# Kernel tuning notes

Hardware: AMD Instinct MI355X
Metric: run time of the kernel (lower is better)

## Reference

```python
import jax, jax.numpy as jnp
from jax import lax
import numpy as np

DIM = 384
NUM_HEADS = 8
HEAD_DIM = DIM // NUM_HEADS


def setup_inputs() -> dict:
    key = jax.random.key(0)
    k_x, k_qw, k_qb, k_lw, k_lb = jax.random.split(key, 5)
    B, H, W = 2, 64, 64
    N = H * W
    x = jax.random.normal(k_x, (B, N, DIM), dtype=jnp.float32)
    # nn.Linear(dim, 3*dim): weight (3C, C), bias (3C,)
    qkv_w = jax.random.normal(k_qw, (3 * DIM, DIM), dtype=jnp.float32) * (1.0 / np.sqrt(DIM))
    qkv_b = jax.random.normal(k_qb, (3 * DIM,), dtype=jnp.float32) * 0.02
    # nn.Conv2d(dim, dim, 3, padding=1, groups=dim): weight (C, 1, 3, 3), bias (C,)
    lepe_w = jax.random.normal(k_lw, (DIM, 1, 3, 3), dtype=jnp.float32) * (1.0 / 3.0)
    lepe_b = jax.random.normal(k_lb, (DIM,), dtype=jnp.float32) * 0.02
    return {"x": x, "qkv_w": qkv_w, "qkv_b": qkv_b, "lepe_w": lepe_w, "lepe_b": lepe_b, "H": H, "W": W}


def reference(x, qkv_w, qkv_b, lepe_w, lepe_b, H, W):
    B, N, C = x.shape
    hd = C // NUM_HEADS
    scale = hd ** -0.5
    # qkv projection: (B, N, 3C) -> (B, N, 3, heads, head_dim)
    qkv = (jnp.einsum('bnc,oc->bno', x, qkv_w) + qkv_b).reshape(B, N, 3, NUM_HEADS, hd)
    q, k, v = qkv[:, :, 0], qkv[:, :, 1], qkv[:, :, 2]  # each (B, N, heads, hd)
    attn = jnp.einsum('bnhd,bmhd->bhnm', q * scale, k)   # (B, heads, N, N)
    attn = jax.nn.softmax(attn, axis=-1)
    out = jnp.einsum('bhnm,bmhd->bnhd', attn, v).reshape(B, N, C)
    # LePE: depthwise 3x3 conv on v in NCHW layout
    v_img = v.reshape(B, H, W, C).transpose(0, 3, 1, 2)  # (B, C, H, W)
    lepe = lax.conv_general_dilated(
        v_img, lepe_w, window_strides=(1, 1), padding='SAME',
        feature_group_count=C,
        dimension_numbers=('NCHW', 'OIHW', 'NCHW'))
    lepe = lepe + lepe_b[None, :, None, None]
    return out + lepe.transpose(0, 2, 3, 1).reshape(B, N, C)
```

## Files before the change

### kernel.cpp

```cpp
#include <hip/hip_runtime.h>
#include <stdint.h>

#define DIM   384
#define NH    8
#define HD    48
#define NTOK  4096
#define KDIM  384
#define SCALEL2E 0.20823509610f

typedef float  f32x4   __attribute__((ext_vector_type(4)));
typedef float  f32x16  __attribute__((ext_vector_type(16)));
typedef __bf16 bf16x8  __attribute__((ext_vector_type(8)));

#if __has_builtin(__builtin_amdgcn_exp2f)
#define EXP2F(x) __builtin_amdgcn_exp2f(x)
#else
#define EXP2F(x) exp2f(x)
#endif

__device__ __forceinline__ unsigned short f2bf(float f) {
  union { float f; unsigned int u; } c; c.f = f;
  unsigned int r = (c.u + 0x7FFFu + ((c.u >> 16) & 1u)) >> 16;
  return (unsigned short)r;
}
__device__ __forceinline__ float bf2f(unsigned short h) {
  union { unsigned int u; float f; } c; c.u = ((unsigned int)h) << 16;
  return c.f;
}


__global__ void prep_kernel(const float* __restrict__ x, const float* __restrict__ w,
                            unsigned short* __restrict__ x_bf,
                            unsigned short* __restrict__ w_bf) {
  int tid = blockIdx.x * blockDim.x + threadIdx.x;
  int stride = gridDim.x * blockDim.x;
  for (int i = tid; i < 786432; i += stride) {
    float4 v = ((const float4*)x)[i];
    ushort4 o;
    o.x = f2bf(v.x); o.y = f2bf(v.y); o.z = f2bf(v.z); o.w = f2bf(v.w);
    ((ushort4*)x_bf)[i] = o;
  }
  for (int i = tid; i < 110592; i += stride) {
    float4 v = ((const float4*)w)[i];
    ushort4 o;
    o.x = f2bf(v.x); o.y = f2bf(v.y); o.z = f2bf(v.z); o.w = f2bf(v.w);
    ((ushort4*)w_bf)[i] = o;
  }
}

__global__ __launch_bounds__(256) void qkv_gemm(
    const unsigned short* __restrict__ A,
    const unsigned short* __restrict__ Bw,
    const float* __restrict__ bias,
    unsigned short* __restrict__ qc,
    unsigned short* __restrict__ kc,
    unsigned short* __restrict__ v_t) {
  __shared__ unsigned short ldsA[128 * 32];
  __shared__ unsigned short ldsB[64 * 32];
  __shared__ unsigned short ebuf[64 * 72];
  const int tid = threadIdx.x;
  const int wv = tid >> 6, ln = tid & 63;
  const int lrow = ln & 15, lq = ln >> 4;
  const int m0 = blockIdx.x * 128;
  const int n0 = blockIdx.y * 64;
  const int wm = (wv >> 1) * 64, wn = (wv & 1) * 32;

  f32x4 acc[4][2];
#pragma unroll
  for (int mi = 0; mi < 4; ++mi)
#pragma unroll
    for (int ni = 0; ni < 2; ++ni)
#pragma unroll
      for (int r = 0; r < 4; ++r) acc[mi][ni][r] = 0.f;

  for (int k0 = 0; k0 < KDIM; k0 += 32) {
    __syncthreads();
#pragma unroll
    for (int j = 0; j < 2; ++j) {
      int r16 = wv * 2 + j;
      const unsigned short* ga = A + (size_t)(m0 + r16 * 16 + (ln >> 2)) * KDIM
                                   + k0 + (ln & 3) * 8;
      __builtin_amdgcn_global_load_lds(
          (const __attribute__((address_space(1))) void*)ga,
          (__attribute__((address_space(3))) void*)&ldsA[r16 * 512], 16, 0, 0);
    }
    const unsigned short* gb = Bw + (size_t)(n0 + wv * 16 + (ln >> 2)) * KDIM
                                  + k0 + (ln & 3) * 8;
    __builtin_amdgcn_global_load_lds(
        (const __attribute__((address_space(1))) void*)gb,
        (__attribute__((address_space(3))) void*)&ldsB[wv * 512], 16, 0, 0);
    __syncthreads();
    bf16x8 af[4], bfv[2];
#pragma unroll
    for (int mi = 0; mi < 4; ++mi)
      af[mi] = *(const bf16x8*)&ldsA[(wm + mi * 16 + lrow) * 32 + lq * 8];
#pragma unroll
    for (int ni = 0; ni < 2; ++ni)
      bfv[ni] = *(const bf16x8*)&ldsB[(wn + ni * 16 + lrow) * 32 + lq * 8];
#pragma unroll
    for (int mi = 0; mi < 4; ++mi)
#pragma unroll
      for (int ni = 0; ni < 2; ++ni)
        acc[mi][ni] = __builtin_amdgcn_mfma_f32_16x16x32_bf16(
            af[mi], bfv[ni], acc[mi][ni], 0, 0, 0);
  }

  const int region = (n0 >= 768) ? 2 : (n0 >= 384 ? 1 : 0);
  const float scl = (region == 0) ? SCALEL2E : 1.0f;
  const float bias0 = bias[n0 + wn + lrow];
  const float bias1 = bias[n0 + wn + 16 + lrow];

#pragma unroll
  for (int half = 0; half < 2; ++half) {
    __syncthreads();
    if ((wv >> 1) == half) {
#pragma unroll
      for (int mi = 0; mi < 4; ++mi)
#pragma unroll
        for (int ni = 0; ni < 2; ++ni)
#pragma unroll
          for (int r = 0; r < 4; ++r) {
            int row = mi * 16 + lq * 4 + r;
            int col = wn + ni * 16 + lrow;
            float val = (acc[mi][ni][r] + (ni ? bias1 : bias0)) * scl;
            ebuf[row * 72 + col] = f2bf(val);
          }
    }
    __syncthreads();
    if (region < 2) {
      unsigned short* dst = (region == 0) ? qc : kc;
      const int obase = n0 - region * 384;
#pragma unroll
      for (int i = 0; i < 2; ++i) {
        int id = tid + i * 256;
        int row = id >> 3, cc = id & 7;
        uint4 val = *(const uint4*)&ebuf[row * 72 + cc * 8];
        int nrow = m0 + half * 64 + row;
        int b = nrow >> 12, nn = nrow & 4095;
        int o = obase + cc * 8;
        int h = o / 48, d = o - h * 48;
        *(uint4*)&dst[((size_t)(b * 8 + h) * NTOK + nn) * HD + d] = val;
      }
    } else {
#pragma unroll
      for (int i = 0; i < 2; ++i) {
        int id = tid + i * 256;
        int col = id & 63, rc = id >> 6;
        int r0 = rc * 8;
        ushort4 lo, hi;
        lo.x = ebuf[(r0 + 0) * 72 + col]; lo.y = ebuf[(r0 + 1) * 72 + col];
        lo.z = ebuf[(r0 + 2) * 72 + col]; lo.w = ebuf[(r0 + 3) * 72 + col];
        hi.x = ebuf[(r0 + 4) * 72 + col]; hi.y = ebuf[(r0 + 5) * 72 + col];
        hi.z = ebuf[(r0 + 6) * 72 + col]; hi.w = ebuf[(r0 + 7) * 72 + col];
        uint4 pk;
        pk.x = (unsigned int)lo.x | ((unsigned int)lo.y << 16);
        pk.y = (unsigned int)lo.z | ((unsigned int)lo.w << 16);
        pk.z = (unsigned int)hi.x | ((unsigned int)hi.y << 16);
        pk.w = (unsigned int)hi.z | ((unsigned int)hi.w << 16);
        int nrow = m0 + half * 64 + r0;
        int b = nrow >> 12;
        int o = n0 - 768 + col;
        *(uint4*)&v_t[((size_t)(b * DIM + o)) * NTOK + (nrow & 4095)] = pk;
      }
    }
  }
}

__global__ __launch_bounds__(256) void lepe_kernel(
    const unsigned short* __restrict__ v_t,
    const float* __restrict__ lw, const float* __restrict__ lb,
    float* __restrict__ out) {
  __shared__ __align__(16) unsigned short pl[16 * 648];
  const int cg = blockIdx.x;
  const int sy = blockIdx.y;
  const int b  = blockIdx.z;
  const int t = threadIdx.x;
  const int y0 = sy * 8;
#pragma unroll
  for (int i = 0; i < 5; ++i) {
    int id = t + i * 256;
    int c = id / 80, rem = id - c * 80;
    int row = rem >> 3, cx = rem & 7;
    int y = y0 - 1 + row;
    uint4 val = make_uint4(0u, 0u, 0u, 0u);
    if (y >= 0 && y < 64)
      val = *(const uint4*)(v_t + ((size_t)(b * DIM + cg * 16 + c)) * NTOK + y * 64 + cx * 8);
    *(uint4*)&pl[c * 648 + row * 64 + cx * 8] = val;
  }
  __syncthreads();
  const int c = t & 15, pg = t >> 4;
  const int cglob = cg * 16 + c;
  float w[9];
#pragma unroll
  for (int j = 0; j < 9; ++j) w[j] = lw[cglob * 9 + j];
  const float bias = lb[cglob];
  const unsigned short* base = &pl[c * 648];
  for (int i = 0; i < 32; ++i) {
    int p = pg * 32 + i;
    int lr = p >> 6, x = p & 63;
    float acc = bias;
#pragma unroll
    for (int ky = 0; ky < 3; ++ky)
#pragma unroll
      for (int kx = 0; kx < 3; ++kx) {
        int xx = x + kx - 1;
        if (xx >= 0 && xx < 64)
          acc += w[ky * 3 + kx] * bf2f(base[(lr + ky) * 64 + xx]);
      }
    out[((size_t)(b * NTOK + sy * 512 + p)) * DIM + cglob] = acc;
  }
}

__global__ __launch_bounds__(256, 2) void attn_kernel(
    const unsigned short* __restrict__ qc,
    const unsigned short* __restrict__ kcg,
    const unsigned short* __restrict__ v_t,
    float* __restrict__ out) {
  __shared__ __align__(16) char smem[36864];
  unsigned short* Kl = (unsigned short*)smem;
  unsigned short* Vl = (unsigned short*)(smem + 18432);
  float* Lsum = (float*)(smem + 35840);
  float* Ol   = (float*)smem;

  const int tid = threadIdx.x;
  const int wv = tid >> 6, ln = tid & 63;
  const int kh = wv >> 1;
  const int wq = wv & 1;
  const int l31 = ln & 31, hh = ln >> 5;
  const int th = tid & 127;
  const int qb = blockIdx.x;
  const int bh = blockIdx.y;
  const int b = bh >> 3, hd = bh & 7;

  unsigned short* Kh = Kl + kh * 4608;
  unsigned short* Vh = Vl + kh * 4352;

  int kwo[4], kgo[4], vwo[3], vgo[3];
#pragma unroll
  for (int i = 0; i < 4; ++i) {
    int idx = th + i * 128;
    int r = idx >> 3, cc = idx & 7;
    kwo[i] = r * 72 + cc * 8;
    kgo[i] = r * 48 + cc * 8;
  }
#pragma unroll
  for (int i = 0; i < 3; ++i) {
    int idx = th + i * 128;
    int vd = idx >> 3, vc = idx & 7;
    vwo[i] = vd * 68 + vc * 8;
    vgo[i] = vd * 4096 + vc * 8;
  }

  if (th < 8) {
    uint4 one4 = make_uint4(0x3F803F80u, 0x3F803F80u, 0x3F803F80u, 0x3F803F80u);
    *(uint4*)&Vh[48 * 68 + th * 8] = one4;
  }

  bf16x8 Qf[2][3];
#pragma unroll
  for (int set = 0; set < 2; ++set) {
    const int qrow = qb * 128 + set * 64 + wq * 32 + l31;
    const unsigned short* qp = qc + ((size_t)bh * NTOK + qrow) * HD + hh * 8;
#pragma unroll
    for (int hs = 0; hs < 3; ++hs)
      Qf[set][hs] = *(const bf16x8*)(qp + hs * 16);
  }

  f32x16 Oacc[2][2];
#pragma unroll
  for (int set = 0; set < 2; ++set)
#pragma unroll
    for (int dc = 0; dc < 2; ++dc)
#pragma unroll
      for (int r = 0; r < 16; ++r) Oacc[set][dc][r] = 0.f;

  const unsigned short* kbase = kcg + (size_t)bh * NTOK * HD;
  const unsigned short* vbase = v_t + ((size_t)b * DIM + hd * HD) * NTOK;

  uint4 kreg0, kreg1, kreg2, kreg3, vreg0, vreg1, vreg2;
  {
    const unsigned short* kg = kbase + (size_t)(kh * 32) * 64 * HD;
    const unsigned short* vg = vbase + (kh * 32) * 64;
    kreg0 = *(const uint4*)(kg + kgo[0]);
    kreg1 = *(const uint4*)(kg + kgo[1]);
    kreg2 = *(const uint4*)(kg + kgo[2]);
    kreg3 = *(const uint4*)(kg + kgo[3]);
    vreg0 = *(const uint4*)(vg + vgo[0]);
    vreg1 = *(const uint4*)(vg + vgo[1]);
    vreg2 = *(const uint4*)(vg + vgo[2]);
  }

  for (int it = 0; it < 32; ++it) {
    __syncthreads();
    *(uint4*)&Kh[kwo[0]] = kreg0;
    *(uint4*)&Kh[kwo[1]] = kreg1;
    *(uint4*)&Kh[kwo[2]] = kreg2;
    *(uint4*)&Kh[kwo[3]] = kreg3;
    *(uint4*)&Vh[vwo[0]] = vreg0;
    *(uint4*)&Vh[vwo[1]] = vreg1;
    *(uint4*)&Vh[vwo[2]] = vreg2;
    {
      int ktn = kh * 32 + ((it + 1) & 31);
      const unsigned short* kg = kbase + (size_t)ktn * 64 * HD;
      const unsigned short* vg = vbase + ktn * 64;
      kreg0 = *(const uint4*)(kg + kgo[0]);
      kreg1 = *(const uint4*)(kg + kgo[1]);
      kreg2 = *(const uint4*)(kg + kgo[2]);
      kreg3 = *(const uint4*)(kg + kgo[3]);
      vreg0 = *(const uint4*)(vg + vgo[0]);
      vreg1 = *(const uint4*)(vg + vgo[1]);
      vreg2 = *(const uint4*)(vg + vgo[2]);
    }
    __syncthreads();

#pragma unroll
    for (int C = 0; C < 2; ++C) {
      f32x16 sA, sB;
#pragma unroll
      for (int r = 0; r < 16; ++r) { sA[r] = 0.f; sB[r] = 0.f; }
      const unsigned short* kr = &Kh[(C * 32 + l31) * 72 + hh * 8];
#pragma unroll
      for (int hs = 0; hs < 3; ++hs) {
        bf16x8 kf = *(const bf16x8*)(kr + hs * 16);
        sA = __builtin_amdgcn_mfma_f32_32x32x16_bf16(kf, Qf[0][hs], sA, 0, 0, 0);
        sB = __builtin_amdgcn_mfma_f32_32x32x16_bf16(kf, Qf[1][hs], sB, 0, 0, 0);
      }
      unsigned int PA[8], PB[8];
#pragma unroll
      for (int t8 = 0; t8 < 8; ++t8) {
        float a0 = EXP2F(sA[2 * t8]);
        float a1 = EXP2F(sA[2 * t8 + 1]);
        PA[t8] = __builtin_amdgcn_perm(__float_as_uint(a1), __float_as_uint(a0),
                                       0x07060302u);
        float b0 = EXP2F(sB[2 * t8]);
        float b1 = EXP2F(sB[2 * t8 + 1]);
        PB[t8] = __builtin_amdgcn_perm(__float_as_uint(b1), __float_as_uint(b0),
                                       0x07060302u);
      }
#pragma unroll
      for (int u = 0; u < 2; ++u) {
        bf16x8 pav0 = __builtin_bit_cast(bf16x8,
            make_uint4(PA[4 * u + 0], PA[4 * u + 1], PA[4 * u + 2], PA[4 * u + 3]));
        bf16x8 pav1 = __builtin_bit_cast(bf16x8,
            make_uint4(PB[4 * u + 0], PB[4 * u + 1], PB[4 * u + 2], PB[4 * u + 3]));
        const int goff = (C * 8 + 4 * u + hh) * 4;
#pragma unroll
        for (int dc = 0; dc < 2; ++dc) {
          const int vrow = dc * 32 + l31;
          const unsigned short* vrp = &Vh[vrow * 68 + goff];
          uint2 g0 = *(const uint2*)(vrp);
          uint2 g2 = *(const uint2*)(vrp + 8);
          bf16x8 vfv = __builtin_bit_cast(bf16x8, make_uint4(g0.x, g0.y, g2.x, g2.y));
          Oacc[0][dc] = __builtin_amdgcn_mfma_f32_32x32x16_bf16(
              pav0, vfv, Oacc[0][dc], 0, 0, 0);
          Oacc[1][dc] = __builtin_amdgcn_mfma_f32_32x32x16_bf16(
              pav1, vfv, Oacc[1][dc], 0, 0, 0);
        }
      }
    }
  }

  __syncthreads();
  if (l31 == 16) {
#pragma unroll
    for (int set = 0; set < 2; ++set)
#pragma unroll
      for (int r = 0; r < 16; ++r) {
        int qrb = set * 64 + wq * 32 + (r & 3) + 8 * (r >> 2) + 4 * hh;
        Lsum[kh * 128 + qrb] = Oacc[set][1][r];
      }
  }
  if (kh == 1) {
#pragma unroll
    for (int set = 0; set < 2; ++set)
#pragma unroll
      for (int r = 0; r < 16; ++r) {
        int qrb = set * 64 + wq * 32 + (r & 3) + 8 * (r >> 2) + 4 * hh;
        Ol[qrb * 48 + l31] = Oacc[set][0][r];
        if (l31 < 16) Ol[qrb * 48 + 32 + l31] = Oacc[set][1][r];
      }
  }
  __syncthreads();
  if (kh == 0) {
#pragma unroll
    for (int set = 0; set < 2; ++set)
#pragma unroll
      for (int r = 0; r < 16; ++r) {
        int qrb = set * 64 + wq * 32 + (r & 3) + 8 * (r >> 2) + 4 * hh;
        float linv = 1.0f / (Lsum[qrb] + Lsum[128 + qrb]);
        float* op = out + ((size_t)(b * NTOK + qb * 128 + qrb)) * DIM + hd * HD;
        op[l31] += (Oacc[set][0][r] + Ol[qrb * 48 + l31]) * linv;
        if (l31 < 16)
          op[32 + l31] += (Oacc[set][1][r] + Ol[qrb * 48 + 32 + l31]) * linv;
      }
  }
}

extern "C" void kernel_launch(void* const* d_in, const int* in_sizes, int n_in,
                              void* d_out, int out_size, void* d_ws, size_t ws_size,
                              hipStream_t stream) {
  const float* x      = (const float*)d_in[0];
  const float* qkv_w  = (const float*)d_in[1];
  const float* qkv_b  = (const float*)d_in[2];
  const float* lepe_w = (const float*)d_in[3];
  const float* lepe_b = (const float*)d_in[4];

  char* ws = (char*)d_ws;
  unsigned short* x_bf = (unsigned short*)(ws);
  unsigned short* w_bf = (unsigned short*)(ws + 6291456);
  unsigned short* qcp  = (unsigned short*)(ws + 7176192);
  unsigned short* kcp  = (unsigned short*)(ws + 13467648);
  unsigned short* v_t  = (unsigned short*)(ws + 19759104);
  float* out = (float*)d_out;

  prep_kernel<<<1024, 256, 0, stream>>>(x, qkv_w, x_bf, w_bf);
  qkv_gemm<<<dim3(64, 18), 256, 0, stream>>>(x_bf, w_bf, qkv_b, qcp, kcp, v_t);
  lepe_kernel<<<dim3(24, 8, 2), 256, 0, stream>>>(v_t, lepe_w, lepe_b, out);
  attn_kernel<<<dim3(32, 16), 256, 0, stream>>>(qcp, kcp, v_t, out);
}
```

Baseline: 188.4 us.

## Split attention KV range across four waves with private LDS tiles

Each attention block now covers 64 queries instead of 128, and the key range is split four ways, one slice per wave. Each wave stages its own 32-key K/V tiles in private LDS, so the per-iteration block barriers are gone. The K tile uses an XOR swizzle to reduce bank conflicts. Row sums now come from accumulating the fp32 exponentials in registers instead of the ones-column MFMA trick, and the four partial outputs are reduced through LDS at the end. The grid doubles and launch bounds ask for 3 blocks per CU. The cost is twice the K/V traffic through L2, plus an extra LDS reduction stage.

```diff
diff --git a/kernel.cpp b/kernel.cpp
--- a/kernel.cpp
+++ b/kernel.cpp
@@ -211,55 +211,45 @@
   }
 }
 
-__global__ __launch_bounds__(256, 2) void attn_kernel(
+__global__ __launch_bounds__(256, 3) void attn_kernel(
     const unsigned short* __restrict__ qc,
     const unsigned short* __restrict__ kcg,
     const unsigned short* __restrict__ v_t,
     float* __restrict__ out) {
-  __shared__ __align__(16) char smem[36864];
+  __shared__ __align__(16) char smem[33056];
   unsigned short* Kl = (unsigned short*)smem;
-  unsigned short* Vl = (unsigned short*)(smem + 18432);
-  float* Lsum = (float*)(smem + 35840);
-  float* Ol   = (float*)smem;
+  unsigned short* Vl = (unsigned short*)(smem + 16384);
+  float* Lsum = (float*)(smem + 32032);
+  float* bufA = (float*)smem;
+  float* bufB = (float*)(smem + 12288);
 
   const int tid = threadIdx.x;
-  const int wv = tid >> 6, ln = tid & 63;
-  const int kh = wv >> 1;
-  const int wq = wv & 1;
+  const int kh = tid >> 6;
+  const int ln = tid & 63;
   const int l31 = ln & 31, hh = ln >> 5;
-  const int th = tid & 127;
   const int qb = blockIdx.x;
   const int bh = blockIdx.y;
   const int b = bh >> 3, hd = bh & 7;
 
-  unsigned short* Kh = Kl + kh * 4608;
-  unsigned short* Vh = Vl + kh * 4352;
-
-  int kwo[4], kgo[4], vwo[3], vgo[3];
-#pragma unroll
-  for (int i = 0; i < 4; ++i) {
-    int idx = th + i * 128;
-    int r = idx >> 3, cc = idx & 7;
-    kwo[i] = r * 72 + cc * 8;
+  unsigned short* Kh = Kl + kh * 2048;
+  unsigned short* Vh = Vl + kh * 1764;
+
+  int kwo[3], kgo[3], vwo[3], vgo[3];
+#pragma unroll
+  for (int i = 0; i < 3; ++i) {
+    int idx = ln + i * 64;
+    int r = idx / 6, cc = idx - r * 6;
+    kwo[i] = r * 64 + ((cc ^ (r & 7)) * 8);
     kgo[i] = r * 48 + cc * 8;
-  }
-#pragma unroll
-  for (int i = 0; i < 3; ++i) {
-    int idx = th + i * 128;
-    int vd = idx >> 3, vc = idx & 7;
-    vwo[i] = vd * 68 + vc * 8;
-    vgo[i] = vd * 4096 + vc * 8;
-  }
-
-  if (th < 8) {
-    uint4 one4 = make_uint4(0x3F803F80u, 0x3F803F80u, 0x3F803F80u, 0x3F803F80u);
-    *(uint4*)&Vh[48 * 68 + th * 8] = one4;
+    int vd = idx >> 2, c4 = idx & 3;
+    vwo[i] = vd * 36 + c4 * 8;
+    vgo[i] = vd * 4096 + c4 * 8;
   }
 
   bf16x8 Qf[2][3];
 #pragma unroll
   for (int set = 0; set < 2; ++set) {
-    const int qrow = qb * 128 + set * 64 + wq * 32 + l31;
+    const int qrow = qb * 64 + set * 32 + l31;
     const unsigned short* qp = qc + ((size_t)bh * NTOK + qrow) * HD + hh * 8;
 #pragma unroll
     for (int hs = 0; hs < 3; ++hs)
@@ -273,112 +263,122 @@
     for (int dc = 0; dc < 2; ++dc)
 #pragma unroll
       for (int r = 0; r < 16; ++r) Oacc[set][dc][r] = 0.f;
+  float lsum0 = 0.f, lsum1 = 0.f;
 
   const unsigned short* kbase = kcg + (size_t)bh * NTOK * HD;
   const unsigned short* vbase = v_t + ((size_t)b * DIM + hd * HD) * NTOK;
 
-  uint4 kreg0, kreg1, kreg2, kreg3, vreg0, vreg1, vreg2;
+  uint4 kr0, kr1, kr2, vr0, vr1, vr2;
   {
-    const unsigned short* kg = kbase + (size_t)(kh * 32) * 64 * HD;
-    const unsigned short* vg = vbase + (kh * 32) * 64;
-    kreg0 = *(const uint4*)(kg + kgo[0]);
-    kreg1 = *(const uint4*)(kg + kgo[1]);
-    kreg2 = *(const uint4*)(kg + kgo[2]);
-    kreg3 = *(const uint4*)(kg + kgo[3]);
-    vreg0 = *(const uint4*)(vg + vgo[0]);
-    vreg1 = *(const uint4*)(vg + vgo[1]);
-    vreg2 = *(const uint4*)(vg + vgo[2]);
+    const unsigned short* kg = kbase + (size_t)(kh * 32) * 32 * HD;
+    const unsigned short* vg = vbase + (kh * 32) * 32;
+    kr0 = *(const uint4*)(kg + kgo[0]);
+    kr1 = *(const uint4*)(kg + kgo[1]);
+    kr2 = *(const uint4*)(kg + kgo[2]);
+    vr0 = *(const uint4*)(vg + vgo[0]);
+    vr1 = *(const uint4*)(vg + vgo[1]);
+    vr2 = *(const uint4*)(vg + vgo[2]);
   }
 
   for (int it = 0; it < 32; ++it) {
-    __syncthreads();
-    *(uint4*)&Kh[kwo[0]] = kreg0;
-    *(uint4*)&Kh[kwo[1]] = kreg1;
-    *(uint4*)&Kh[kwo[2]] = kreg2;
-    *(uint4*)&Kh[kwo[3]] = kreg3;
-    *(uint4*)&Vh[vwo[0]] = vreg0;
-    *(uint4*)&Vh[vwo[1]] = vreg1;
-    *(uint4*)&Vh[vwo[2]] = vreg2;
+    *(uint4*)&Kh[kwo[0]] = kr0;
+    *(uint4*)&Kh[kwo[1]] = kr1;
+    *(uint4*)&Kh[kwo[2]] = kr2;
+    *(uint4*)&Vh[vwo[0]] = vr0;
+    *(uint4*)&Vh[vwo[1]] = vr1;
+    *(uint4*)&Vh[vwo[2]] = vr2;
     {
       int ktn = kh * 32 + ((it + 1) & 31);
-      const unsigned short* kg = kbase + (size_t)ktn * 64 * HD;
-      const unsigned short* vg = vbase + ktn * 64;
-      kreg0 = *(const uint4*)(kg + kgo[0]);
-      kreg1 = *(const uint4*)(kg + kgo[1]);
-      kreg2 = *(const uint4*)(kg + kgo[2]);
-      kreg3 = *(const uint4*)(kg + kgo[3]);
-      vreg0 = *(const uint4*)(vg + vgo[0]);
-      vreg1 = *(const uint4*)(vg + vgo[1]);
-      vreg2 = *(const uint4*)(vg + vgo[2]);
-    }
-    __syncthreads();
-
-#pragma unroll
-    for (int C = 0; C < 2; ++C) {
-      f32x16 sA, sB;
-#pragma unroll
-      for (int r = 0; r < 16; ++r) { sA[r] = 0.f; sB[r] = 0.f; }
-      const unsigned short* kr = &Kh[(C * 32 + l31) * 72 + hh * 8];
-#pragma unroll
-      for (int hs = 0; hs < 3; ++hs) {
-        bf16x8 kf = *(const bf16x8*)(kr + hs * 16);
-        sA = __builtin_amdgcn_mfma_f32_32x32x16_bf16(kf, Qf[0][hs], sA, 0, 0, 0);
-        sB = __builtin_amdgcn_mfma_f32_32x32x16_bf16(kf, Qf[1][hs], sB, 0, 0, 0);
+      const unsigned short* kg = kbase + (size_t)ktn * 32 * HD;
+      const unsigned short* vg = vbase + ktn * 32;
+      kr0 = *(const uint4*)(kg + kgo[0]);
+      kr1 = *(const uint4*)(kg + kgo[1]);
+      kr2 = *(const uint4*)(kg + kgo[2]);
+      vr0 = *(const uint4*)(vg + vgo[0]);
+      vr1 = *(const uint4*)(vg + vgo[1]);
+      vr2 = *(const uint4*)(vg + vgo[2]);
+    }
+
+    f32x16 sA, sB;
+#pragma unroll
+    for (int r = 0; r < 16; ++r) { sA[r] = 0.f; sB[r] = 0.f; }
+    const unsigned short* kr = &Kh[l31 * 64];
+    const int rx = l31 & 7;
+#pragma unroll
+    for (int hs = 0; hs < 3; ++hs) {
+      bf16x8 kf = *(const bf16x8*)&kr[((hs * 2 + hh) ^ rx) * 8];
+      sA = __builtin_amdgcn_mfma_f32_32x32x16_bf16(kf, Qf[0][hs], sA, 0, 0, 0);
+      sB = __builtin_amdgcn_mfma_f32_32x32x16_bf16(kf, Qf[1][hs], sB, 0, 0, 0);
+    }
+    unsigned int PA[8], PB[8];
+#pragma unroll
+    for (int t8 = 0; t8 < 8; ++t8) {
+      float a0 = EXP2F(sA[2 * t8]);
+      float a1 = EXP2F(sA[2 * t8 + 1]);
+      lsum0 += a0 + a1;
+      PA[t8] = __builtin_amdgcn_perm(__float_as_uint(a1), __float_as_uint(a0),
+                                     0x07060302u);
+      float b0 = EXP2F(sB[2 * t8]);
+      float b1 = EXP2F(sB[2 * t8 + 1]);
+      lsum1 += b0 + b1;
+      PB[t8] = __builtin_amdgcn_perm(__float_as_uint(b1), __float_as_uint(b0),
+                                     0x07060302u);
+    }
+#pragma unroll
+    for (int u = 0; u < 2; ++u) {
+      bf16x8 pav0 = __builtin_bit_cast(bf16x8,
+          make_uint4(PA[4 * u + 0], PA[4 * u + 1], PA[4 * u + 2], PA[4 * u + 3]));
+      bf16x8 pav1 = __builtin_bit_cast(bf16x8,
+          make_uint4(PB[4 * u + 0], PB[4 * u + 1], PB[4 * u + 2], PB[4 * u + 3]));
+      const int goff = (4 * u + hh) * 4;
+#pragma unroll
+      for (int dc = 0; dc < 2; ++dc) {
+        const int vrow = dc * 32 + l31;
+        const unsigned short* vrp = &Vh[vrow * 36 + goff];
+        uint2 g0 = *(const uint2*)(vrp);
+        uint2 g2 = *(const uint2*)(vrp + 8);
+        bf16x8 vfv = __builtin_bit_cast(bf16x8, make_uint4(g0.x, g0.y, g2.x, g2.y));
+        Oacc[0][dc] = __builtin_amdgcn_mfma_f32_32x32x16_bf16(
+            pav0, vfv, Oacc[0][dc], 0, 0, 0);
+        Oacc[1][dc] = __builtin_amdgcn_mfma_f32_32x32x16_bf16(
+            pav1, vfv, Oacc[1][dc], 0, 0, 0);
       }
-      unsigned int PA[8], PB[8];
-#pragma unroll
-      for (int t8 = 0; t8 < 8; ++t8) {
-        float a0 = EXP2F(sA[2 * t8]);
-        float a1 = EXP2F(sA[2 * t8 + 1]);
-        PA[t8] = __builtin_amdgcn_perm(__float_as_uint(a1), __float_as_uint(a0),
-                                       0x07060302u);
-        float b0 = EXP2F(sB[2 * t8]);
-        float b1 = EXP2F(sB[2 * t8 + 1]);
-        PB[t8] = __builtin_amdgcn_perm(__float_as_uint(b1), __float_as_uint(b0),
-                                       0x07060302u);
-      }
-#pragma unroll
-      for (int u = 0; u < 2; ++u) {
-        bf16x8 pav0 = __builtin_bit_cast(bf16x8,
-            make_uint4(PA[4 * u + 0], PA[4 * u + 1], PA[4 * u + 2], PA[4 * u + 3]));
-        bf16x8 pav1 = __builtin_bit_cast(bf16x8,
-            make_uint4(PB[4 * u + 0], PB[4 * u + 1], PB[4 * u + 2], PB[4 * u + 3]));
-        const int goff = (C * 8 + 4 * u + hh) * 4;
-#pragma unroll
-        for (int dc = 0; dc < 2; ++dc) {
-          const int vrow = dc * 32 + l31;
-          const unsigned short* vrp = &Vh[vrow * 68 + goff];
-          uint2 g0 = *(const uint2*)(vrp);
-          uint2 g2 = *(const uint2*)(vrp + 8);
-          bf16x8 vfv = __builtin_bit_cast(bf16x8, make_uint4(g0.x, g0.y, g2.x, g2.y));
-          Oacc[0][dc] = __builtin_amdgcn_mfma_f32_32x32x16_bf16(
-              pav0, vfv, Oacc[0][dc], 0, 0, 0);
-          Oacc[1][dc] = __builtin_amdgcn_mfma_f32_32x32x16_bf16(
-              pav1, vfv, Oacc[1][dc], 0, 0, 0);
+    }
+  }
+
+  float ls0 = lsum0 + __shfl_xor(lsum0, 32, 64);
+  float ls1 = lsum1 + __shfl_xor(lsum1, 32, 64);
+  __syncthreads();
+  if (ln < 32) {
+    Lsum[kh * 64 + ln] = ls0;
+    Lsum[kh * 64 + 32 + ln] = ls1;
+  }
+  if ((kh & 1) == 0) {
+    float* buf = (kh == 0) ? bufA : bufB;
+#pragma unroll
+    for (int set = 0; set < 2; ++set)
+#pragma unroll
+      for (int dc = 0; dc < 2; ++dc)
+#pragma unroll
+        for (int r = 0; r < 16; ++r) {
+          int qrow = set * 32 + (r & 3) + 8 * (r >> 2) + 4 * hh;
+          int d = dc * 32 + l31;
+          if (d < HD) buf[qrow * 48 + d] = Oacc[set][dc][r];
         }
-      }
-    }
-  }
-
+  }
   __syncthreads();
-  if (l31 == 16) {
+  if ((kh & 1) == 1) {
+    float* buf = (kh == 1) ? bufA : bufB;
 #pragma unroll
     for (int set = 0; set < 2; ++set)
 #pragma unroll
-      for (int r = 0; r < 16; ++r) {
-        int qrb = set * 64 + wq * 32 + (r & 3) + 8 * (r >> 2) + 4 * hh;
-        Lsum[kh * 128 + qrb] = Oacc[set][1][r];
-      }
-  }
-  if (kh == 1) {
-#pragma unroll
-    for (int set = 0; set < 2; ++set)
-#pragma unroll
-      for (int r = 0; r < 16; ++r) {
-        int qrb = set * 64 + wq * 32 + (r & 3) + 8 * (r >> 2) + 4 * hh;
-        Ol[qrb * 48 + l31] = Oacc[set][0][r];
-        if (l31 < 16) Ol[qrb * 48 + 32 + l31] = Oacc[set][1][r];
-      }
+      for (int dc = 0; dc < 2; ++dc)
+#pragma unroll
+        for (int r = 0; r < 16; ++r) {
+          int qrow = set * 32 + (r & 3) + 8 * (r >> 2) + 4 * hh;
+          int d = dc * 32 + l31;
+          if (d < HD) buf[qrow * 48 + d] += Oacc[set][dc][r];
+        }
   }
   __syncthreads();
   if (kh == 0) {
@@ -386,12 +386,13 @@
     for (int set = 0; set < 2; ++set)
 #pragma unroll
       for (int r = 0; r < 16; ++r) {
-        int qrb = set * 64 + wq * 32 + (r & 3) + 8 * (r >> 2) + 4 * hh;
-        float linv = 1.0f / (Lsum[qrb] + Lsum[128 + qrb]);
-        float* op = out + ((size_t)(b * NTOK + qb * 128 + qrb)) * DIM + hd * HD;
-        op[l31] += (Oacc[set][0][r] + Ol[qrb * 48 + l31]) * linv;
+        int qrow = set * 32 + (r & 3) + 8 * (r >> 2) + 4 * hh;
+        float lt = Lsum[qrow] + Lsum[64 + qrow] + Lsum[128 + qrow] + Lsum[192 + qrow];
+        float linv = 1.0f / lt;
+        float* op = out + ((size_t)(b * NTOK + qb * 64 + qrow)) * DIM + hd * HD;
+        op[l31] += (bufA[qrow * 48 + l31] + bufB[qrow * 48 + l31]) * linv;
         if (l31 < 16)
-          op[32 + l31] += (Oacc[set][1][r] + Ol[qrb * 48 + 32 + l31]) * linv;
+          op[32 + l31] += (bufA[qrow * 48 + 32 + l31] + bufB[qrow * 48 + 32 + l31]) * linv;
       }
   }
 }
@@ -416,5 +417,5 @@
   prep_kernel<<<1024, 256, 0, stream>>>(x, qkv_w, x_bf, w_bf);
   qkv_gemm<<<dim3(64, 18), 256, 0, stream>>>(x_bf, w_bf, qkv_b, qcp, kcp, v_t);
   lepe_kernel<<<dim3(24, 8, 2), 256, 0, stream>>>(v_t, lepe_w, lepe_b, out);
-  attn_kernel<<<dim3(32, 16), 256, 0, stream>>>(qcp, kcp, v_t, out);
-}
+  attn_kernel<<<dim3(64, 16), 256, 0, stream>>>(qcp, kcp, v_t, out);
+}
```

After: 279.8 us. 1.48x slower.
